# Optimization experiments

Measured on AMD Instinct MI355X. Metric: run time of the kernel, lower is better.

## Reference

```python
import jax, jax.numpy as jnp
import numpy as np

B, S, D, H = 2, 2048, 1024, 16
HD = D // H  # head_dim = 64


def setup_inputs() -> dict:
    key = jax.random.key(0)
    ks = jax.random.split(key, 8)
    std = 1.0 / np.sqrt(D)
    return {
        "q": jax.random.normal(ks[0], (B, S, D), jnp.float32),
        "k": jax.random.normal(ks[1], (B, S, D), jnp.float32),
        "v": jax.random.normal(ks[2], (B, S, D), jnp.float32),
        "attn_mask": jnp.ones((B, S, S), jnp.int32),
        "Wq": jax.random.normal(ks[3], (D, D), jnp.float32) * std,
        "bq": jnp.zeros((D,), jnp.float32),
        "Wk": jax.random.normal(ks[4], (D, D), jnp.float32) * std,
        "bk": jnp.zeros((D,), jnp.float32),
        "Wv": jax.random.normal(ks[5], (D, D), jnp.float32) * std,
        "bv": jnp.zeros((D,), jnp.float32),
        "Wo": jax.random.normal(ks[6], (D, D), jnp.float32) * std,
        "bo": jnp.zeros((D,), jnp.float32),
    }


def reference(q, k, v, attn_mask, Wq, bq, Wk, bk, Wv, bv, Wo, bo):
    # Linear projections (torch Linear: x @ W.T + b; here W stored as [in, out])
    Q = q @ Wq + bq
    K = k @ Wk + bk
    V = v @ Wv + bv
    # split heads: [B, H, S, HD]
    def split(x):
        return x.reshape(B, S, H, HD).transpose(0, 2, 1, 3)
    q_s, k_s, v_s = split(Q), split(K), split(V)
    # NOTE: original code calls scores.masked_fill(...) NON-in-place and
    # discards the result, so attn_mask has NO effect on the math.
    scale = 1.0 / np.sqrt(HD).astype(np.float32)
    scores = jnp.einsum("bhqd,bhkd->bhqk", q_s, k_s) * scale  # [B,H,S,S]
    attn = jax.nn.softmax(scores, axis=-1)
    context = jnp.einsum("bhqk,bhkd->bhqd", attn, v_s)
    context = context.transpose(0, 2, 1, 3).reshape(B, S, D)
    out = context @ Wo + bo
    return (out, attn)
```

## Files before the change

kernel.cpp:

```cpp
#include <hip/hip_runtime.h>
#include <hip/hip_bf16.h>

typedef __bf16 bf16;
typedef bf16 v8bf __attribute__((ext_vector_type(8)));
typedef bf16 v4bf __attribute__((ext_vector_type(4)));
typedef float v4f __attribute__((ext_vector_type(4)));

constexpr int Bc = 2, Sc = 2048, Dc = 1024, Hc = 16, HDc = 64;
constexpr int Mr = Bc * Sc;

__device__ inline v4f mfma16(v8bf a, v8bf b, v4f c) {
    return __builtin_amdgcn_mfma_f32_16x16x32_bf16(a, b, c, 0, 0, 0);
}

__device__ inline void gload_lds16(const void* g, void* l) {
    __builtin_amdgcn_global_load_lds((__attribute__((address_space(1))) void*)g,
                                     (__attribute__((address_space(3))) void*)l, 16, 0, 0);
}

__global__ void wtrans_kernel(const float* __restrict__ Wq, const float* __restrict__ Wk,
                              const float* __restrict__ Wv, const float* __restrict__ Wo,
                              bf16* __restrict__ out) {
    __shared__ float t[32][33];
    const float* W = (blockIdx.z == 0) ? Wq : (blockIdx.z == 1) ? Wk : (blockIdx.z == 2) ? Wv : Wo;
    bf16* Wt = out + (size_t)blockIdx.z * (Dc * Dc);
    int x0 = blockIdx.x * 32, y0 = blockIdx.y * 32;
    int tx = threadIdx.x, ty = threadIdx.y;
#pragma unroll
    for (int i = 0; i < 4; i++)
        t[ty + 8 * i][tx] = W[(size_t)(y0 + ty + 8 * i) * Dc + x0 + tx];
    __syncthreads();
#pragma unroll
    for (int i = 0; i < 4; i++)
        Wt[(size_t)(x0 + ty + 8 * i) * Dc + y0 + tx] = (bf16)t[tx][ty + 8 * i];
}

__global__ void cvt_kernel(const float* __restrict__ in, bf16* __restrict__ out) {
    size_t i = ((size_t)blockIdx.x * blockDim.x + threadIdx.x) * 8;
    float4 f0 = *(const float4*)(in + i);
    float4 f1 = *(const float4*)(in + i + 4);
    v8bf v;
    v[0] = (bf16)f0.x; v[1] = (bf16)f0.y; v[2] = (bf16)f0.z; v[3] = (bf16)f0.w;
    v[4] = (bf16)f1.x; v[5] = (bf16)f1.y; v[6] = (bf16)f1.z; v[7] = (bf16)f1.w;
    *(v8bf*)(out + i) = v;
}

__global__ void vtrans_kernel(const bf16* __restrict__ V, bf16* __restrict__ Vt) {
    __shared__ bf16 t[32][33];
    int b = blockIdx.z;
    const bf16* Vb = V + (size_t)b * Sc * Dc;
    bf16* Vtb = Vt + (size_t)b * Dc * Sc;
    int s0 = blockIdx.x * 32, d0 = blockIdx.y * 32;
    int tx = threadIdx.x, ty = threadIdx.y;
#pragma unroll
    for (int i = 0; i < 4; i++)
        t[ty + 8 * i][tx] = Vb[(size_t)(s0 + ty + 8 * i) * Dc + d0 + tx];
    __syncthreads();
#pragma unroll
    for (int i = 0; i < 4; i++)
        Vtb[(size_t)(d0 + ty + 8 * i) * Sc + s0 + tx] = t[tx][ty + 8 * i];
}

template <typename TOut>
__global__ __launch_bounds__(256) void gemm_kernel(const bf16* __restrict__ X,
                                                   const bf16* __restrict__ Wt,
                                                   const float* __restrict__ bias,
                                                   TOut* __restrict__ Y) {
    __shared__ bf16 As[128][64];
    __shared__ bf16 Bs[64][64];
    const int mTile = blockIdx.x * 128, nTile = blockIdx.y * 64;
    const int tid = threadIdx.x;
    const int w = tid >> 6, l = tid & 63, lr = l & 15, quad = l >> 4;
    const int wm = w & 1, wn = w >> 1;
    const int srow = l >> 3, scol = (l & 7) * 8;

    v4f acc[4][2];
#pragma unroll
    for (int mt = 0; mt < 4; mt++)
#pragma unroll
        for (int nt = 0; nt < 2; nt++) acc[mt][nt] = v4f{0.f, 0.f, 0.f, 0.f};

    float bv[2];
#pragma unroll
    for (int nt = 0; nt < 2; nt++) bv[nt] = bias[nTile + wn * 32 + nt * 16 + lr];

    const bf16* Xbase = X + (size_t)mTile * Dc;
    const bf16* Wbase = Wt + (size_t)nTile * Dc;

    for (int kt = 0; kt < Dc; kt += 64) {
        __syncthreads();
#pragma unroll
        for (int i = 0; i < 4; i++) {
            int r = w * 32 + i * 8 + srow;
            gload_lds16(Xbase + (size_t)r * Dc + kt + scol, &As[w * 32 + i * 8][0]);
        }
#pragma unroll
        for (int i = 0; i < 2; i++) {
            int r = w * 16 + i * 8 + srow;
            gload_lds16(Wbase + (size_t)r * Dc + kt + scol, &Bs[w * 16 + i * 8][0]);
        }
        __syncthreads();

        v8bf a[4][2], bb[2][2];
#pragma unroll
        for (int mt = 0; mt < 4; mt++)
#pragma unroll
            for (int kk = 0; kk < 2; kk++)
                a[mt][kk] = *(const v8bf*)&As[wm * 64 + mt * 16 + lr][kk * 32 + quad * 8];
#pragma unroll
        for (int nt = 0; nt < 2; nt++)
#pragma unroll
            for (int kk = 0; kk < 2; kk++)
                bb[nt][kk] = *(const v8bf*)&Bs[wn * 32 + nt * 16 + lr][kk * 32 + quad * 8];
#pragma unroll
        for (int kk = 0; kk < 2; kk++)
#pragma unroll
            for (int mt = 0; mt < 4; mt++)
#pragma unroll
                for (int nt = 0; nt < 2; nt++)
                    acc[mt][nt] = mfma16(a[mt][kk], bb[nt][kk], acc[mt][nt]);
    }

#pragma unroll
    for (int mt = 0; mt < 4; mt++)
#pragma unroll
        for (int nt = 0; nt < 2; nt++)
#pragma unroll
            for (int r = 0; r < 4; r++) {
                int row = mTile + wm * 64 + mt * 16 + quad * 4 + r;
                int col = nTile + wn * 32 + nt * 16 + lr;
                Y[(size_t)row * Dc + col] = (TOut)(acc[mt][nt][r] + bv[nt]);
            }
}

__global__ __launch_bounds__(256) void attn_kernel(const bf16* __restrict__ Q,
                                                   const bf16* __restrict__ K,
                                                   const bf16* __restrict__ Vt,
                                                   float* __restrict__ attn,
                                                   bf16* __restrict__ ctx) {
    __shared__ bf16 Ps[4][16][40];
    const int b = blockIdx.z, h = blockIdx.y, rb = blockIdx.x;
    const int tid = threadIdx.x, w = tid >> 6, l = tid & 63, lr = l & 15, quad = l >> 4;
    const int r0 = rb * 64 + w * 16;
    const float scale = 0.125f;

    const bf16* Qrow = Q + (size_t)(b * Sc + r0 + lr) * Dc + h * HDc;
    v8bf qa0 = *(const v8bf*)(Qrow + quad * 8);
    v8bf qa1 = *(const v8bf*)(Qrow + 32 + quad * 8);

    const bf16* Kbase = K + (size_t)(b * Sc) * Dc + h * HDc;

    float sum = 0.f, sumB = 0.f;
    for (int ct = 0; ct < Sc / 16; ct += 2) {
        const bf16* Kr0 = Kbase + (size_t)(ct * 16 + lr) * Dc;
        const bf16* Kr1 = Kr0 + 16 * Dc;
        v8bf k00 = *(const v8bf*)(Kr0 + quad * 8);
        v8bf k01 = *(const v8bf*)(Kr0 + 32 + quad * 8);
        v8bf k10 = *(const v8bf*)(Kr1 + quad * 8);
        v8bf k11 = *(const v8bf*)(Kr1 + 32 + quad * 8);
        v4f s0 = v4f{0.f, 0.f, 0.f, 0.f}, s1 = v4f{0.f, 0.f, 0.f, 0.f};
        s0 = mfma16(k00, qa0, s0);
        s0 = mfma16(k01, qa1, s0);
        s1 = mfma16(k10, qa0, s1);
        s1 = mfma16(k11, qa1, s1);
#pragma unroll
        for (int r = 0; r < 4; r++) sum += __expf(s0[r] * scale);
#pragma unroll
        for (int r = 0; r < 4; r++) sumB += __expf(s1[r] * scale);
    }
    sum += sumB;
    sum += __shfl_xor(sum, 16);
    sum += __shfl_xor(sum, 32);
    const float inv = 1.0f / sum;

    float* attnRow = attn + ((size_t)((b * Hc + h) * Sc + r0 + lr)) * Sc;
    const bf16* VtBase = Vt + (size_t)(b * Dc + h * HDc) * Sc;

    v4f acc[4];
#pragma unroll
    for (int nt = 0; nt < 4; nt++) acc[nt] = v4f{0.f, 0.f, 0.f, 0.f};

    constexpr int NT = Sc / 32;
    v8bf k00, k01, k10, k11, vb[4];
    {
        const bf16* Kr0 = Kbase + (size_t)lr * Dc;
        const bf16* Kr1 = Kr0 + 16 * Dc;
        k00 = *(const v8bf*)(Kr0 + quad * 8);
        k01 = *(const v8bf*)(Kr0 + 32 + quad * 8);
        k10 = *(const v8bf*)(Kr1 + quad * 8);
        k11 = *(const v8bf*)(Kr1 + 32 + quad * 8);
#pragma unroll
        for (int nt = 0; nt < 4; nt++)
            vb[nt] = *(const v8bf*)(VtBase + (size_t)(nt * 16 + lr) * Sc + quad * 8);
    }

    for (int ctp = 0; ctp < NT; ctp++) {
        v4f s0 = v4f{0.f, 0.f, 0.f, 0.f}, s1 = v4f{0.f, 0.f, 0.f, 0.f};
        s0 = mfma16(k00, qa0, s0);
        s0 = mfma16(k01, qa1, s0);
        s1 = mfma16(k10, qa0, s1);
        s1 = mfma16(k11, qa1, s1);

        const int nc = (ctp + 1 < NT) ? ctp + 1 : ctp;
        const bf16* Kr0n = Kbase + (size_t)(nc * 32 + lr) * Dc;
        const bf16* Kr1n = Kr0n + 16 * Dc;
        v8bf n00 = *(const v8bf*)(Kr0n + quad * 8);
        v8bf n01 = *(const v8bf*)(Kr0n + 32 + quad * 8);
        v8bf n10 = *(const v8bf*)(Kr1n + quad * 8);
        v8bf n11 = *(const v8bf*)(Kr1n + 32 + quad * 8);
        v8bf vn[4];
#pragma unroll
        for (int nt = 0; nt < 4; nt++)
            vn[nt] = *(const v8bf*)(VtBase + (size_t)(nt * 16 + lr) * Sc + nc * 32 + quad * 8);

        v4f p0, p1;
        v4bf pb0, pb1;
#pragma unroll
        for (int r = 0; r < 4; r++) {
            p0[r] = __expf(s0[r] * scale) * inv;
            pb0[r] = (bf16)p0[r];
        }
#pragma unroll
        for (int r = 0; r < 4; r++) {
            p1[r] = __expf(s1[r] * scale) * inv;
            pb1[r] = (bf16)p1[r];
        }
        __builtin_nontemporal_store(p0, (v4f*)(attnRow + ctp * 32 + quad * 4));
        __builtin_nontemporal_store(p1, (v4f*)(attnRow + ctp * 32 + 16 + quad * 4));
        *(v4bf*)&Ps[w][lr][quad * 4] = pb0;
        *(v4bf*)&Ps[w][lr][16 + quad * 4] = pb1;
        asm volatile("s_waitcnt lgkmcnt(0)" ::: "memory");
        __builtin_amdgcn_sched_barrier(0);
        v8bf pa = *(const v8bf*)&Ps[w][lr][quad * 8];
#pragma unroll
        for (int nt = 0; nt < 4; nt++) acc[nt] = mfma16(pa, vb[nt], acc[nt]);

        k00 = n00; k01 = n01; k10 = n10; k11 = n11;
#pragma unroll
        for (int nt = 0; nt < 4; nt++) vb[nt] = vn[nt];
    }

#pragma unroll
    for (int nt = 0; nt < 4; nt++)
#pragma unroll
        for (int r = 0; r < 4; r++) {
            size_t row = (size_t)(b * Sc + r0 + quad * 4 + r);
            ctx[row * Dc + h * HDc + nt * 16 + lr] = (bf16)acc[nt][r];
        }
}

extern "C" void kernel_launch(void* const* d_in, const int* in_sizes, int n_in,
                              void* d_out, int out_size, void* d_ws, size_t ws_size,
                              hipStream_t stream) {
    const float* q  = (const float*)d_in[0];
    const float* k  = (const float*)d_in[1];
    const float* v  = (const float*)d_in[2];
    const float* Wq = (const float*)d_in[4];
    const float* bq = (const float*)d_in[5];
    const float* Wk = (const float*)d_in[6];
    const float* bk = (const float*)d_in[7];
    const float* Wv = (const float*)d_in[8];
    const float* bv = (const float*)d_in[9];
    const float* Wo = (const float*)d_in[10];
    const float* bo = (const float*)d_in[11];

    char* ws = (char*)d_ws;
    const size_t MB8 = 8388608;
    bf16* T0  = (bf16*)(ws);
    bf16* Qbf = (bf16*)(ws + 1 * MB8);
    bf16* Kbf = (bf16*)(ws + 2 * MB8);
    bf16* Vbf = (bf16*)(ws + 3 * MB8);
    bf16* Vt  = (bf16*)(ws + 4 * MB8);
    bf16* Wts = (bf16*)(ws + 5 * MB8);
    bf16* Wqt = Wts;
    bf16* Wkt = Wts + 1 * (size_t)(Dc * Dc);
    bf16* Wvt = Wts + 2 * (size_t)(Dc * Dc);
    bf16* Wot = Wts + 3 * (size_t)(Dc * Dc);
    bf16* ctx = Vbf;

    float* outp = (float*)d_out;
    float* attn = outp + (size_t)Mr * Dc;

    wtrans_kernel<<<dim3(32, 32, 4), dim3(32, 8), 0, stream>>>(Wq, Wk, Wv, Wo, Wts);

    cvt_kernel<<<dim3(2048), 256, 0, stream>>>(q, T0);
    gemm_kernel<bf16><<<dim3(32, 16), 256, 0, stream>>>(T0, Wqt, bq, Qbf);
    cvt_kernel<<<dim3(2048), 256, 0, stream>>>(k, T0);
    gemm_kernel<bf16><<<dim3(32, 16), 256, 0, stream>>>(T0, Wkt, bk, Kbf);
    cvt_kernel<<<dim3(2048), 256, 0, stream>>>(v, T0);
    gemm_kernel<bf16><<<dim3(32, 16), 256, 0, stream>>>(T0, Wvt, bv, Vbf);

    vtrans_kernel<<<dim3(64, 32, 2), dim3(32, 8), 0, stream>>>(Vbf, Vt);
    attn_kernel<<<dim3(32, 16, 2), 256, 0, stream>>>(Qbf, Kbf, Vt, attn, ctx);
    gemm_kernel<float><<<dim3(32, 16), 256, 0, stream>>>(ctx, Wot, bo, outp);
}
```

Baseline: 972.6 us.

## Swizzle GEMM LDS, double-buffer attention K/V loads, drop LDS P transpose

The GEMM's LDS tiles get an XOR swizzle on column offsets to cut bank conflicts on the fragment reads. The attention kernel now prefetches K (and V) two groups ahead using alternating A/B register buffers in both passes. It also replaces the LDS round trip for P with 16x16x16 bf16 MFMAs that take the exp output directly as the A operand. The attn stores change from nontemporal to normal stores, which may raise cache pressure, and the extra register buffers may reduce occupancy.

```diff
diff --git a/kernel.cpp b/kernel.cpp
--- a/kernel.cpp
+++ b/kernel.cpp
@@ -4,6 +4,7 @@
 typedef __bf16 bf16;
 typedef bf16 v8bf __attribute__((ext_vector_type(8)));
 typedef bf16 v4bf __attribute__((ext_vector_type(4)));
+typedef short v4s __attribute__((ext_vector_type(4)));
 typedef float v4f __attribute__((ext_vector_type(4)));
 
 constexpr int Bc = 2, Sc = 2048, Dc = 1024, Hc = 16, HDc = 64;
@@ -11,6 +12,19 @@
 
 __device__ inline v4f mfma16(v8bf a, v8bf b, v4f c) {
     return __builtin_amdgcn_mfma_f32_16x16x32_bf16(a, b, c, 0, 0, 0);
+}
+
+__device__ inline v4f mfma16x16(v4bf a, v4bf b, v4f c) {
+#if __has_builtin(__builtin_amdgcn_mfma_f32_16x16x16bf16_1k)
+    v4s as, bs;
+    __builtin_memcpy(&as, &a, 8);
+    __builtin_memcpy(&bs, &b, 8);
+    return __builtin_amdgcn_mfma_f32_16x16x16bf16_1k(as, bs, c, 0, 0, 0);
+#else
+    asm volatile("s_nop 1\n\tv_mfma_f32_16x16x16_bf16 %0, %1, %2, %0"
+                 : "+v"(c) : "v"(a), "v"(b));
+    return c;
+#endif
 }
 
 __device__ inline void gload_lds16(const void* g, void* l) {
@@ -72,7 +86,8 @@
     const int tid = threadIdx.x;
     const int w = tid >> 6, l = tid & 63, lr = l & 15, quad = l >> 4;
     const int wm = w & 1, wn = w >> 1;
-    const int srow = l >> 3, scol = (l & 7) * 8;
+    const int srow = l >> 3;
+    const int selem = ((l & 7) * 8) ^ (srow << 3);
 
     v4f acc[4][2];
 #pragma unroll
@@ -86,18 +101,19 @@
 
     const bf16* Xbase = X + (size_t)mTile * Dc;
     const bf16* Wbase = Wt + (size_t)nTile * Dc;
+    const int swzA = (lr & 7) << 3;
 
     for (int kt = 0; kt < Dc; kt += 64) {
         __syncthreads();
 #pragma unroll
         for (int i = 0; i < 4; i++) {
             int r = w * 32 + i * 8 + srow;
-            gload_lds16(Xbase + (size_t)r * Dc + kt + scol, &As[w * 32 + i * 8][0]);
+            gload_lds16(Xbase + (size_t)r * Dc + kt + selem, &As[w * 32 + i * 8][0]);
         }
 #pragma unroll
         for (int i = 0; i < 2; i++) {
             int r = w * 16 + i * 8 + srow;
-            gload_lds16(Wbase + (size_t)r * Dc + kt + scol, &Bs[w * 16 + i * 8][0]);
+            gload_lds16(Wbase + (size_t)r * Dc + kt + selem, &Bs[w * 16 + i * 8][0]);
         }
         __syncthreads();
 
@@ -106,12 +122,12 @@
         for (int mt = 0; mt < 4; mt++)
 #pragma unroll
             for (int kk = 0; kk < 2; kk++)
-                a[mt][kk] = *(const v8bf*)&As[wm * 64 + mt * 16 + lr][kk * 32 + quad * 8];
+                a[mt][kk] = *(const v8bf*)&As[wm * 64 + mt * 16 + lr][(kk * 32 + quad * 8) ^ swzA];
 #pragma unroll
         for (int nt = 0; nt < 2; nt++)
 #pragma unroll
             for (int kk = 0; kk < 2; kk++)
-                bb[nt][kk] = *(const v8bf*)&Bs[wn * 32 + nt * 16 + lr][kk * 32 + quad * 8];
+                bb[nt][kk] = *(const v8bf*)&Bs[wn * 32 + nt * 16 + lr][(kk * 32 + quad * 8) ^ swzA];
 #pragma unroll
         for (int kk = 0; kk < 2; kk++)
 #pragma unroll
@@ -133,40 +149,76 @@
             }
 }
 
+struct KF { v8bf f0, f1, f2, f3; };
+__device__ inline KF loadKF(const bf16* base, int key0, int lr, int quad) {
+    KF r;
+    const bf16* p0 = base + (size_t)(key0 + lr) * Dc;
+    const bf16* p1 = p0 + 16 * Dc;
+    r.f0 = *(const v8bf*)(p0 + quad * 8);
+    r.f1 = *(const v8bf*)(p0 + 32 + quad * 8);
+    r.f2 = *(const v8bf*)(p1 + quad * 8);
+    r.f3 = *(const v8bf*)(p1 + 32 + quad * 8);
+    return r;
+}
+struct VF { v4bf a0, a1, a2, a3, b0, b1, b2, b3; };
+__device__ inline VF loadVF(const bf16* vt, int key0, int lr, int quad) {
+    VF r;
+    const bf16* p = vt + key0 + quad * 4;
+    r.a0 = *(const v4bf*)(p + (size_t)(0 * 16 + lr) * Sc);
+    r.a1 = *(const v4bf*)(p + (size_t)(1 * 16 + lr) * Sc);
+    r.a2 = *(const v4bf*)(p + (size_t)(2 * 16 + lr) * Sc);
+    r.a3 = *(const v4bf*)(p + (size_t)(3 * 16 + lr) * Sc);
+    r.b0 = *(const v4bf*)(p + 16 + (size_t)(0 * 16 + lr) * Sc);
+    r.b1 = *(const v4bf*)(p + 16 + (size_t)(1 * 16 + lr) * Sc);
+    r.b2 = *(const v4bf*)(p + 16 + (size_t)(2 * 16 + lr) * Sc);
+    r.b3 = *(const v4bf*)(p + 16 + (size_t)(3 * 16 + lr) * Sc);
+    return r;
+}
+
 __global__ __launch_bounds__(256) void attn_kernel(const bf16* __restrict__ Q,
                                                    const bf16* __restrict__ K,
                                                    const bf16* __restrict__ Vt,
                                                    float* __restrict__ attn,
                                                    bf16* __restrict__ ctx) {
-    __shared__ bf16 Ps[4][16][40];
     const int b = blockIdx.z, h = blockIdx.y, rb = blockIdx.x;
     const int tid = threadIdx.x, w = tid >> 6, l = tid & 63, lr = l & 15, quad = l >> 4;
     const int r0 = rb * 64 + w * 16;
     const float scale = 0.125f;
+    constexpr int NG = Sc / 32;
 
     const bf16* Qrow = Q + (size_t)(b * Sc + r0 + lr) * Dc + h * HDc;
     v8bf qa0 = *(const v8bf*)(Qrow + quad * 8);
     v8bf qa1 = *(const v8bf*)(Qrow + 32 + quad * 8);
 
     const bf16* Kbase = K + (size_t)(b * Sc) * Dc + h * HDc;
+    const bf16* VtBase = Vt + (size_t)(b * Dc + h * HDc) * Sc;
 
     float sum = 0.f, sumB = 0.f;
-    for (int ct = 0; ct < Sc / 16; ct += 2) {
-        const bf16* Kr0 = Kbase + (size_t)(ct * 16 + lr) * Dc;
-        const bf16* Kr1 = Kr0 + 16 * Dc;
-        v8bf k00 = *(const v8bf*)(Kr0 + quad * 8);
-        v8bf k01 = *(const v8bf*)(Kr0 + 32 + quad * 8);
-        v8bf k10 = *(const v8bf*)(Kr1 + quad * 8);
-        v8bf k11 = *(const v8bf*)(Kr1 + 32 + quad * 8);
-        v4f s0 = v4f{0.f, 0.f, 0.f, 0.f}, s1 = v4f{0.f, 0.f, 0.f, 0.f};
-        s0 = mfma16(k00, qa0, s0);
-        s0 = mfma16(k01, qa1, s0);
-        s1 = mfma16(k10, qa0, s1);
-        s1 = mfma16(k11, qa1, s1);
-#pragma unroll
-        for (int r = 0; r < 4; r++) sum += __expf(s0[r] * scale);
-#pragma unroll
-        for (int r = 0; r < 4; r++) sumB += __expf(s1[r] * scale);
+    KF kA = loadKF(Kbase, 0, lr, quad);
+    KF kB = loadKF(Kbase, 32, lr, quad);
+    for (int g = 0; g < NG; g += 2) {
+        {
+            v4f s0 = v4f{0.f, 0.f, 0.f, 0.f}, s1 = v4f{0.f, 0.f, 0.f, 0.f};
+            s0 = mfma16(kA.f0, qa0, s0); s0 = mfma16(kA.f1, qa1, s0);
+            s1 = mfma16(kA.f2, qa0, s1); s1 = mfma16(kA.f3, qa1, s1);
+            int ng = (g + 2 < NG) ? g + 2 : g;
+            kA = loadKF(Kbase, ng * 32, lr, quad);
+#pragma unroll
+            for (int r = 0; r < 4; r++) sum += __expf(s0[r] * scale);
+#pragma unroll
+            for (int r = 0; r < 4; r++) sumB += __expf(s1[r] * scale);
+        }
+        {
+            v4f s0 = v4f{0.f, 0.f, 0.f, 0.f}, s1 = v4f{0.f, 0.f, 0.f, 0.f};
+            s0 = mfma16(kB.f0, qa0, s0); s0 = mfma16(kB.f1, qa1, s0);
+            s1 = mfma16(kB.f2, qa0, s1); s1 = mfma16(kB.f3, qa1, s1);
+            int ng = (g + 3 < NG) ? g + 3 : g + 1;
+            kB = loadKF(Kbase, ng * 32, lr, quad);
+#pragma unroll
+            for (int r = 0; r < 4; r++) sum += __expf(s0[r] * scale);
+#pragma unroll
+            for (int r = 0; r < 4; r++) sumB += __expf(s1[r] * scale);
+        }
     }
     sum += sumB;
     sum += __shfl_xor(sum, 16);
@@ -174,71 +226,62 @@
     const float inv = 1.0f / sum;
 
     float* attnRow = attn + ((size_t)((b * Hc + h) * Sc + r0 + lr)) * Sc;
-    const bf16* VtBase = Vt + (size_t)(b * Dc + h * HDc) * Sc;
 
     v4f acc[4];
 #pragma unroll
     for (int nt = 0; nt < 4; nt++) acc[nt] = v4f{0.f, 0.f, 0.f, 0.f};
 
-    constexpr int NT = Sc / 32;
-    v8bf k00, k01, k10, k11, vb[4];
-    {
-        const bf16* Kr0 = Kbase + (size_t)lr * Dc;
-        const bf16* Kr1 = Kr0 + 16 * Dc;
-        k00 = *(const v8bf*)(Kr0 + quad * 8);
-        k01 = *(const v8bf*)(Kr0 + 32 + quad * 8);
-        k10 = *(const v8bf*)(Kr1 + quad * 8);
-        k11 = *(const v8bf*)(Kr1 + 32 + quad * 8);
-#pragma unroll
-        for (int nt = 0; nt < 4; nt++)
-            vb[nt] = *(const v8bf*)(VtBase + (size_t)(nt * 16 + lr) * Sc + quad * 8);
+    KF k2A = loadKF(Kbase, 0, lr, quad);
+    VF v2A = loadVF(VtBase, 0, lr, quad);
+    KF k2B = loadKF(Kbase, 32, lr, quad);
+    VF v2B = loadVF(VtBase, 32, lr, quad);
+
+    for (int g = 0; g < NG; g += 2) {
+        {
+            v4f s0 = v4f{0.f, 0.f, 0.f, 0.f}, s1 = v4f{0.f, 0.f, 0.f, 0.f};
+            s0 = mfma16(k2A.f0, qa0, s0); s0 = mfma16(k2A.f1, qa1, s0);
+            s1 = mfma16(k2A.f2, qa0, s1); s1 = mfma16(k2A.f3, qa1, s1);
+            int ng = (g + 2 < NG) ? g + 2 : g;
+            KF nk = loadKF(Kbase, ng * 32, lr, quad);
+            VF nv = loadVF(VtBase, ng * 32, lr, quad);
+            v4f p0, p1;
+            v4bf pb0, pb1;
+#pragma unroll
+            for (int r = 0; r < 4; r++) { p0[r] = __expf(s0[r] * scale) * inv; pb0[r] = (bf16)p0[r]; }
+#pragma unroll
+            for (int r = 0; r < 4; r++) { p1[r] = __expf(s1[r] * scale) * inv; pb1[r] = (bf16)p1[r]; }
+            *(v4f*)(attnRow + g * 32 + quad * 4) = p0;
+            *(v4f*)(attnRow + g * 32 + 16 + quad * 4) = p1;
+            acc[0] = mfma16x16(pb0, v2A.a0, acc[0]); acc[1] = mfma16x16(pb0, v2A.a1, acc[1]);
+            acc[2] = mfma16x16(pb0, v2A.a2, acc[2]); acc[3] = mfma16x16(pb0, v2A.a3, acc[3]);
+            acc[0] = mfma16x16(pb1, v2A.b0, acc[0]); acc[1] = mfma16x16(pb1, v2A.b1, acc[1]);
+            acc[2] = mfma16x16(pb1, v2A.b2, acc[2]); acc[3] = mfma16x16(pb1, v2A.b3, acc[3]);
+            k2A = nk; v2A = nv;
+        }
+        {
+            v4f s0 = v4f{0.f, 0.f, 0.f, 0.f}, s1 = v4f{0.f, 0.f, 0.f, 0.f};
+            s0 = mfma16(k2B.f0, qa0, s0); s0 = mfma16(k2B.f1, qa1, s0);
+            s1 = mfma16(k2B.f2, qa0, s1); s1 = mfma16(k2B.f3, qa1, s1);
+            int ng = (g + 3 < NG) ? g + 3 : g + 1;
+            KF nk = loadKF(Kbase, ng * 32, lr, quad);
+            VF nv = loadVF(VtBase, ng * 32, lr, quad);
+            v4f p0, p1;
+            v4bf pb0, pb1;
+#pragma unroll
+            for (int r = 0; r < 4; r++) { p0[r] = __expf(s0[r] * scale) * inv; pb0[r] = (bf16)p0[r]; }
+#pragma unroll
+            for (int r = 0; r < 4; r++) { p1[r] = __expf(s1[r] * scale) * inv; pb1[r] = (bf16)p1[r]; }
+            *(v4f*)(attnRow + (g + 1) * 32 + quad * 4) = p0;
+            *(v4f*)(attnRow + (g + 1) * 32 + 16 + quad * 4) = p1;
+            acc[0] = mfma16x16(pb0, v2B.a0, acc[0]); acc[1] = mfma16x16(pb0, v2B.a1, acc[1]);
+            acc[2] = mfma16x16(pb0, v2B.a2, acc[2]); acc[3] = mfma16x16(pb0, v2B.a3, acc[3]);
+            acc[0] = mfma16x16(pb1, v2B.b0, acc[0]); acc[1] = mfma16x16(pb1, v2B.b1, acc[1]);
+            acc[2] = mfma16x16(pb1, v2B.b2, acc[2]); acc[3] = mfma16x16(pb1, v2B.b3, acc[3]);
+            k2B = nk; v2B = nv;
+        }
     }
 
-    for (int ctp = 0; ctp < NT; ctp++) {
-        v4f s0 = v4f{0.f, 0.f, 0.f, 0.f}, s1 = v4f{0.f, 0.f, 0.f, 0.f};
-        s0 = mfma16(k00, qa0, s0);
-        s0 = mfma16(k01, qa1, s0);
-        s1 = mfma16(k10, qa0, s1);
-        s1 = mfma16(k11, qa1, s1);
-
-        const int nc = (ctp + 1 < NT) ? ctp + 1 : ctp;
-        const bf16* Kr0n = Kbase + (size_t)(nc * 32 + lr) * Dc;
-        const bf16* Kr1n = Kr0n + 16 * Dc;
-        v8bf n00 = *(const v8bf*)(Kr0n + quad * 8);
-        v8bf n01 = *(const v8bf*)(Kr0n + 32 + quad * 8);
-        v8bf n10 = *(const v8bf*)(Kr1n + quad * 8);
-        v8bf n11 = *(const v8bf*)(Kr1n + 32 + quad * 8);
-        v8bf vn[4];
-#pragma unroll
-        for (int nt = 0; nt < 4; nt++)
-            vn[nt] = *(const v8bf*)(VtBase + (size_t)(nt * 16 + lr) * Sc + nc * 32 + quad * 8);
-
-        v4f p0, p1;
-        v4bf pb0, pb1;
-#pragma unroll
-        for (int r = 0; r < 4; r++) {
-            p0[r] = __expf(s0[r] * scale) * inv;
-            pb0[r] = (bf16)p0[r];
-        }
-#pragma unroll
-        for (int r = 0; r < 4; r++) {
-            p1[r] = __expf(s1[r] * scale) * inv;
-            pb1[r] = (bf16)p1[r];
-        }
-        __builtin_nontemporal_store(p0, (v4f*)(attnRow + ctp * 32 + quad * 4));
-        __builtin_nontemporal_store(p1, (v4f*)(attnRow + ctp * 32 + 16 + quad * 4));
-        *(v4bf*)&Ps[w][lr][quad * 4] = pb0;
-        *(v4bf*)&Ps[w][lr][16 + quad * 4] = pb1;
-        asm volatile("s_waitcnt lgkmcnt(0)" ::: "memory");
-        __builtin_amdgcn_sched_barrier(0);
-        v8bf pa = *(const v8bf*)&Ps[w][lr][quad * 8];
-#pragma unroll
-        for (int nt = 0; nt < 4; nt++) acc[nt] = mfma16(pa, vb[nt], acc[nt]);
-
-        k00 = n00; k01 = n01; k10 = n10; k11 = n11;
-#pragma unroll
-        for (int nt = 0; nt < 4; nt++) vb[nt] = vn[nt];
-    }
+    asm volatile("s_nop 7" :::);
 
 #pragma unroll
     for (int nt = 0; nt < 4; nt++)
```

Result: slower. 1.103 ms (+13.4%).

## Double-buffer and swizzle GEMM LDS, batch Q/K projections, shrink attention blocks

Applied to the files above, without the earlier changes.

The GEMM now double-buffers its LDS tiles with async global-to-LDS loads, waiting on vmcnt so the next tile loads during compute. It XOR-swizzles the LDS column layout to reduce bank conflicts. The Q and K projections run as one batched launch over blockIdx.z, which relies on slotA/slotB and Wq/Wk being contiguous in the workspace. The attention kernel drops from 4 waves to 1 wave per block with 4x more blocks, and swaps nontemporal attn stores for regular stores, changing occupancy and cache behaviour.

```diff
diff --git a/kernel.cpp b/kernel.cpp
--- a/kernel.cpp
+++ b/kernel.cpp
@@ -62,17 +62,25 @@
 }
 
 template <typename TOut>
-__global__ __launch_bounds__(256) void gemm_kernel(const bf16* __restrict__ X,
-                                                   const bf16* __restrict__ Wt,
-                                                   const float* __restrict__ bias,
-                                                   TOut* __restrict__ Y) {
-    __shared__ bf16 As[128][64];
-    __shared__ bf16 Bs[64][64];
+__global__ __launch_bounds__(256) void gemm_kernel(const bf16* __restrict__ X0,
+                                                   const bf16* __restrict__ W0,
+                                                   const float* __restrict__ bias0,
+                                                   const float* __restrict__ bias1,
+                                                   TOut* __restrict__ Y0) {
+    __shared__ bf16 As[2][128][64];
+    __shared__ bf16 Bs[2][64][64];
+    const int z = blockIdx.z;
+    const bf16* X = X0 + (size_t)z * Mr * Dc;
+    const bf16* Wt = W0 + (size_t)z * Dc * Dc;
+    const float* bias = z ? bias1 : bias0;
+    TOut* Y = Y0 + (size_t)z * Mr * Dc;
+
     const int mTile = blockIdx.x * 128, nTile = blockIdx.y * 64;
     const int tid = threadIdx.x;
     const int w = tid >> 6, l = tid & 63, lr = l & 15, quad = l >> 4;
     const int wm = w & 1, wn = w >> 1;
-    const int srow = l >> 3, scol = (l & 7) * 8;
+    const int srow = l >> 3;
+    const int scol = ((l & 7) * 8) ^ (srow << 3);
 
     v4f acc[4][2];
 #pragma unroll
@@ -86,32 +94,45 @@
 
     const bf16* Xbase = X + (size_t)mTile * Dc;
     const bf16* Wbase = Wt + (size_t)nTile * Dc;
-
-    for (int kt = 0; kt < Dc; kt += 64) {
-        __syncthreads();
-#pragma unroll
-        for (int i = 0; i < 4; i++) {
-            int r = w * 32 + i * 8 + srow;
-            gload_lds16(Xbase + (size_t)r * Dc + kt + scol, &As[w * 32 + i * 8][0]);
+    const int swzA = (lr & 7) << 3;
+
+#define STAGE(buf, kt)                                                                  \
+    {                                                                                   \
+        _Pragma("unroll") for (int i = 0; i < 4; i++)                                   \
+            gload_lds16(Xbase + (size_t)(w * 32 + i * 8 + srow) * Dc + (kt) + scol,     \
+                        &As[buf][w * 32 + i * 8][0]);                                   \
+        _Pragma("unroll") for (int i = 0; i < 2; i++)                                   \
+            gload_lds16(Wbase + (size_t)(w * 16 + i * 8 + srow) * Dc + (kt) + scol,     \
+                        &Bs[buf][w * 16 + i * 8][0]);                                   \
+    }
+
+    STAGE(0, 0);
+    for (int s = 0; s < 16; s++) {
+        const int cur = s & 1;
+        if (s < 15) {
+            STAGE(cur ^ 1, (s + 1) * 64);
+            __builtin_amdgcn_sched_barrier(0);
+            asm volatile("s_waitcnt vmcnt(6)" ::: "memory");
+        } else {
+            __builtin_amdgcn_sched_barrier(0);
+            asm volatile("s_waitcnt vmcnt(0)" ::: "memory");
         }
-#pragma unroll
-        for (int i = 0; i < 2; i++) {
-            int r = w * 16 + i * 8 + srow;
-            gload_lds16(Wbase + (size_t)r * Dc + kt + scol, &Bs[w * 16 + i * 8][0]);
-        }
-        __syncthreads();
+        __builtin_amdgcn_s_barrier();
+        __builtin_amdgcn_sched_barrier(0);
 
         v8bf a[4][2], bb[2][2];
 #pragma unroll
         for (int mt = 0; mt < 4; mt++)
 #pragma unroll
             for (int kk = 0; kk < 2; kk++)
-                a[mt][kk] = *(const v8bf*)&As[wm * 64 + mt * 16 + lr][kk * 32 + quad * 8];
+                a[mt][kk] =
+                    *(const v8bf*)&As[cur][wm * 64 + mt * 16 + lr][(kk * 32 + quad * 8) ^ swzA];
 #pragma unroll
         for (int nt = 0; nt < 2; nt++)
 #pragma unroll
             for (int kk = 0; kk < 2; kk++)
-                bb[nt][kk] = *(const v8bf*)&Bs[wn * 32 + nt * 16 + lr][kk * 32 + quad * 8];
+                bb[nt][kk] =
+                    *(const v8bf*)&Bs[cur][wn * 32 + nt * 16 + lr][(kk * 32 + quad * 8) ^ swzA];
 #pragma unroll
         for (int kk = 0; kk < 2; kk++)
 #pragma unroll
@@ -119,7 +140,11 @@
 #pragma unroll
                 for (int nt = 0; nt < 2; nt++)
                     acc[mt][nt] = mfma16(a[mt][kk], bb[nt][kk], acc[mt][nt]);
-    }
+
+        __builtin_amdgcn_sched_barrier(0);
+        __builtin_amdgcn_s_barrier();
+    }
+#undef STAGE
 
 #pragma unroll
     for (int mt = 0; mt < 4; mt++)
@@ -133,15 +158,15 @@
             }
 }
 
-__global__ __launch_bounds__(256) void attn_kernel(const bf16* __restrict__ Q,
-                                                   const bf16* __restrict__ K,
-                                                   const bf16* __restrict__ Vt,
-                                                   float* __restrict__ attn,
-                                                   bf16* __restrict__ ctx) {
-    __shared__ bf16 Ps[4][16][40];
+__global__ __launch_bounds__(64) void attn_kernel(const bf16* __restrict__ Q,
+                                                  const bf16* __restrict__ K,
+                                                  const bf16* __restrict__ Vt,
+                                                  float* __restrict__ attn,
+                                                  bf16* __restrict__ ctx) {
+    __shared__ bf16 Ps[16][40];
     const int b = blockIdx.z, h = blockIdx.y, rb = blockIdx.x;
-    const int tid = threadIdx.x, w = tid >> 6, l = tid & 63, lr = l & 15, quad = l >> 4;
-    const int r0 = rb * 64 + w * 16;
+    const int l = threadIdx.x & 63, lr = l & 15, quad = l >> 4;
+    const int r0 = rb * 16;
     const float scale = 0.125f;
 
     const bf16* Qrow = Q + (size_t)(b * Sc + r0 + lr) * Dc + h * HDc;
@@ -216,22 +241,16 @@
         v4f p0, p1;
         v4bf pb0, pb1;
 #pragma unroll
-        for (int r = 0; r < 4; r++) {
-            p0[r] = __expf(s0[r] * scale) * inv;
-            pb0[r] = (bf16)p0[r];
-        }
-#pragma unroll
-        for (int r = 0; r < 4; r++) {
-            p1[r] = __expf(s1[r] * scale) * inv;
-            pb1[r] = (bf16)p1[r];
-        }
-        __builtin_nontemporal_store(p0, (v4f*)(attnRow + ctp * 32 + quad * 4));
-        __builtin_nontemporal_store(p1, (v4f*)(attnRow + ctp * 32 + 16 + quad * 4));
-        *(v4bf*)&Ps[w][lr][quad * 4] = pb0;
-        *(v4bf*)&Ps[w][lr][16 + quad * 4] = pb1;
+        for (int r = 0; r < 4; r++) { p0[r] = __expf(s0[r] * scale) * inv; pb0[r] = (bf16)p0[r]; }
+#pragma unroll
+        for (int r = 0; r < 4; r++) { p1[r] = __expf(s1[r] * scale) * inv; pb1[r] = (bf16)p1[r]; }
+        *(v4f*)(attnRow + ctp * 32 + quad * 4) = p0;
+        *(v4f*)(attnRow + ctp * 32 + 16 + quad * 4) = p1;
+        *(v4bf*)&Ps[lr][quad * 4] = pb0;
+        *(v4bf*)&Ps[lr][16 + quad * 4] = pb1;
         asm volatile("s_waitcnt lgkmcnt(0)" ::: "memory");
         __builtin_amdgcn_sched_barrier(0);
-        v8bf pa = *(const v8bf*)&Ps[w][lr][quad * 8];
+        v8bf pa = *(const v8bf*)&Ps[lr][quad * 8];
 #pragma unroll
         for (int nt = 0; nt < 4; nt++) acc[nt] = mfma16(pa, vb[nt], acc[nt]);
 
@@ -266,31 +285,28 @@
 
     char* ws = (char*)d_ws;
     const size_t MB8 = 8388608;
-    bf16* T0  = (bf16*)(ws);
-    bf16* Qbf = (bf16*)(ws + 1 * MB8);
-    bf16* Kbf = (bf16*)(ws + 2 * MB8);
-    bf16* Vbf = (bf16*)(ws + 3 * MB8);
-    bf16* Vt  = (bf16*)(ws + 4 * MB8);
-    bf16* Wts = (bf16*)(ws + 5 * MB8);
-    bf16* Wqt = Wts;
-    bf16* Wkt = Wts + 1 * (size_t)(Dc * Dc);
+    bf16* slotA = (bf16*)(ws + 0 * MB8);
+    bf16* slotB = (bf16*)(ws + 1 * MB8);
+    bf16* Wts   = (bf16*)(ws + 2 * MB8);
+    bf16* Qbf   = (bf16*)(ws + 3 * MB8);
+    bf16* Kbf   = (bf16*)(ws + 4 * MB8);
+    bf16* Vbf   = (bf16*)(ws + 5 * MB8);
     bf16* Wvt = Wts + 2 * (size_t)(Dc * Dc);
     bf16* Wot = Wts + 3 * (size_t)(Dc * Dc);
-    bf16* ctx = Vbf;
 
     float* outp = (float*)d_out;
     float* attn = outp + (size_t)Mr * Dc;
 
     wtrans_kernel<<<dim3(32, 32, 4), dim3(32, 8), 0, stream>>>(Wq, Wk, Wv, Wo, Wts);
 
-    cvt_kernel<<<dim3(2048), 256, 0, stream>>>(q, T0);
-    gemm_kernel<bf16><<<dim3(32, 16), 256, 0, stream>>>(T0, Wqt, bq, Qbf);
-    cvt_kernel<<<dim3(2048), 256, 0, stream>>>(k, T0);
-    gemm_kernel<bf16><<<dim3(32, 16), 256, 0, stream>>>(T0, Wkt, bk, Kbf);
-    cvt_kernel<<<dim3(2048), 256, 0, stream>>>(v, T0);
-    gemm_kernel<bf16><<<dim3(32, 16), 256, 0, stream>>>(T0, Wvt, bv, Vbf);
-
-    vtrans_kernel<<<dim3(64, 32, 2), dim3(32, 8), 0, stream>>>(Vbf, Vt);
-    attn_kernel<<<dim3(32, 16, 2), 256, 0, stream>>>(Qbf, Kbf, Vt, attn, ctx);
-    gemm_kernel<float><<<dim3(32, 16), 256, 0, stream>>>(ctx, Wot, bo, outp);
-}
+    cvt_kernel<<<dim3(2048), 256, 0, stream>>>(q, slotA);
+    cvt_kernel<<<dim3(2048), 256, 0, stream>>>(k, slotB);
+    gemm_kernel<bf16><<<dim3(32, 16, 2), 256, 0, stream>>>(slotA, Wts, bq, bk, Qbf);
+
+    cvt_kernel<<<dim3(2048), 256, 0, stream>>>(v, slotA);
+    gemm_kernel<bf16><<<dim3(32, 16, 1), 256, 0, stream>>>(slotA, Wvt, bv, bv, Vbf);
+
+    vtrans_kernel<<<dim3(64, 32, 2), dim3(32, 8), 0, stream>>>(Vbf, slotB);
+    attn_kernel<<<dim3(128, 16, 2), 64, 0, stream>>>(Qbf, Kbf, slotB, attn, slotA);
+    gemm_kernel<float><<<dim3(32, 16, 1), 256, 0, stream>>>(slotA, Wot, bo, bo, outp);
+}
```

Result: no change. 986.2 us (+1.4%).
